# Optimization experiments

Hardware: AMD Instinct MI355X
Metric: run time of the kernel (lower is better)

Reference implementation:

```python
import math
import jax, jax.numpy as jnp
import numpy as np

B, N, D, H = 4, 2048, 1024, 16
DK = D // H

def setup_inputs() -> dict:
    key = jax.random.key(0)
    k1, k2, k3 = jax.random.split(key, 3)
    x = jax.random.normal(k1, (B, N, D), dtype=jnp.float32)
    # torch Linear weight is [out,in]; we store transposed [in,out] for x @ W
    w_qkv = jax.random.normal(k2, (D, 3 * D), dtype=jnp.float32) * (1.0 / math.sqrt(D))
    w_out = jax.random.normal(k3, (D, D), dtype=jnp.float32) * (1.0 / math.sqrt(D))
    return {"x": x, "w_qkv": w_qkv, "w_out": w_out}

def reference(x, w_qkv, w_out):
    b, n, d = x.shape
    qkv = x @ w_qkv                                   # [B,N,3D]
    q, k, v = jnp.split(qkv, 3, axis=-1)
    def split_heads(t):
        return t.reshape(b, n, H, DK).transpose(0, 2, 1, 3)  # [B,H,N,DK]
    q, k, v = map(split_heads, (q, k, v))
    scale = 1.0 / math.sqrt(DK)
    attn = jnp.einsum('bhqd,bhkd->bhqk', q, k) * scale  # [B,H,N,N]
    attn = jax.nn.softmax(attn, axis=-1)
    out = jnp.einsum('bhqk,bhkd->bhqd', attn, v)        # [B,H,N,DK]
    out = out.transpose(0, 2, 1, 3).reshape(b, n, d)
    return out @ w_out                                  # dropout p=0 -> identity
```

## Files before the change

### kernel.cpp

```cpp
#include <hip/hip_runtime.h>
#include <hip/hip_bf16.h>

typedef __bf16 bf16;
typedef __bf16 bf16x8 __attribute__((ext_vector_type(8)));
typedef float f32x2 __attribute__((ext_vector_type(2)));
typedef float f32x4 __attribute__((ext_vector_type(4)));
typedef float f32x16 __attribute__((ext_vector_type(16)));
typedef short s16x4 __attribute__((ext_vector_type(4)));

#define GLDS16(gp, lp) __builtin_amdgcn_global_load_lds( \
    (const __attribute__((address_space(1))) void*)(gp), \
    (__attribute__((address_space(3))) void*)(lp), 16, 0, 0)

__device__ __forceinline__ bf16 f2bf(float f) {
    unsigned u = __builtin_bit_cast(unsigned, f);
    u = (u + 0x7FFFu + ((u >> 16) & 1u)) >> 16;
    unsigned short s = (unsigned short)u;
    return __builtin_bit_cast(bf16, s);
}
__device__ __forceinline__ void store_c(float* p, float v) { *p = v; }
__device__ __forceinline__ void store_c(bf16*  p, float v) { *p = f2bf(v); }

__device__ __forceinline__ float exp2_fast(float x) {
    float r; asm("v_exp_f32 %0, %1" : "=v"(r) : "v"(x)); return r;
}
__device__ __forceinline__ unsigned cvt_pk_bf16(float lo, float hi) {
    unsigned r;
    asm("v_cvt_pk_bf16_f32 %0, %1, %2" : "=v"(r) : "v"(lo), "v"(hi));
    return r;
}
__device__ __forceinline__ void permlane32_swap(unsigned &a, unsigned &b) {
    asm("v_permlane32_swap_b32 %0, %1" : "+v"(a), "+v"(b));
}
__device__ __forceinline__ s16x4 ds_tr16(unsigned addr) {
    s16x4 d;
    asm volatile("ds_read_b64_tr_b16 %0, %1" : "=v"(d) : "v"(addr));
    return d;
}

__global__ __launch_bounds__(256) void cvt_f32_bf16(
    const float* __restrict__ in, bf16* __restrict__ out, int n8)
{
    int i = blockIdx.x * 256 + threadIdx.x;
    if (i >= n8) return;
    f32x4 a = *(const f32x4*)(in + (size_t)i * 8);
    f32x4 b = *(const f32x4*)(in + (size_t)i * 8 + 4);
    bf16x8 o;
    #pragma unroll
    for (int j = 0; j < 4; ++j) { o[j] = f2bf(a[j]); o[4 + j] = f2bf(b[j]); }
    *(bf16x8*)(out + (size_t)i * 8) = o;
}

template <typename TC>
__global__ __launch_bounds__(256) void gemm_glds(
    const bf16* __restrict__ A, const bf16* __restrict__ B, TC* __restrict__ C,
    int M, int N, int K)
{
    __shared__ alignas(16) bf16 As[128 * 32];
    __shared__ alignas(16) bf16 Bs[32 * 128];

    const int tid  = threadIdx.x;
    const int wv   = tid >> 6;
    const int lane = tid & 63;
    const int lr   = lane & 15;
    const int kb   = lane >> 4;
    const int wr   = wv >> 1, wc = wv & 1;
    const int brow = blockIdx.y * 128;
    const int bcol = blockIdx.x * 128;

    f32x4 acc[4][4] = {};

    const int ar0 = wv * 16 + (lane >> 2);
    const int ac0 = (lane & 3) * 8;

    const int bL   = wv * 1024 + lane * 16;
    const int bs0  = bL >> 7;
    const int b_r  = (bL & 127) >> 5;
    const int b_c0 = (bL & 31) >> 1;

    for (int k0 = 0; k0 < K; k0 += 32) {
        __syncthreads();
        #pragma unroll
        for (int t = 0; t < 2; ++t)
            GLDS16(A + (size_t)(brow + t * 64 + ar0) * K + k0 + ac0,
                   &As[t * 2048 + wv * 512]);
        #pragma unroll
        for (int t = 0; t < 2; ++t) {
            int s = bs0 + t * 32;
            GLDS16(B + (size_t)(k0 + (s >> 3) * 4 + b_r) * N + bcol + (s & 7) * 16 + b_c0,
                   &Bs[t * 2048 + wv * 512]);
        }
        __syncthreads();

        bf16x8 af[4], bfr[4];
        #pragma unroll
        for (int m = 0; m < 4; ++m)
            af[m] = *(const bf16x8*)&As[(wr * 64 + m * 16 + lr) * 32 + kb * 8];
        {
            s16x4 tr[8];
            const unsigned bsb = (unsigned)(uintptr_t)Bs + kb * 2048 + lr * 8;
            #pragma unroll
            for (int nt = 0; nt < 4; ++nt) {
                unsigned a = bsb + (wc * 4 + nt) * 128;
                tr[nt * 2]     = ds_tr16(a);
                tr[nt * 2 + 1] = ds_tr16(a + 1024);
            }
            asm volatile("s_waitcnt lgkmcnt(0)" ::: "memory");
            __builtin_amdgcn_sched_barrier(0);
            #pragma unroll
            for (int nt = 0; nt < 4; ++nt) {
                union { bf16x8 f; s16x4 h[2]; } u;
                u.h[0] = tr[nt * 2]; u.h[1] = tr[nt * 2 + 1];
                bfr[nt] = u.f;
            }
        }
        #pragma unroll
        for (int m = 0; m < 4; ++m)
            #pragma unroll
            for (int n = 0; n < 4; ++n)
                acc[m][n] = __builtin_amdgcn_mfma_f32_16x16x32_bf16(af[m], bfr[n], acc[m][n], 0, 0, 0);
    }

    #pragma unroll
    for (int m = 0; m < 4; ++m)
        #pragma unroll
        for (int n = 0; n < 4; ++n)
            #pragma unroll
            for (int r = 0; r < 4; ++r) {
                int row = brow + wr * 64 + m * 16 + kb * 4 + r;
                int col = bcol + wc * 64 + n * 16 + lr;
                store_c(&C[(size_t)row * N + col], acc[m][n][r]);
            }
}

__global__ __launch_bounds__(256) void attn_mfma32(
    const bf16* __restrict__ qkv, bf16* __restrict__ attn_out)
{
    constexpr int NSEQ = 2048, DM = 1024, LD = 3072, KVB = 64, QB = 128;
    constexpr int NT = NSEQ / KVB;
    constexpr float THR = 11.5f;
    __shared__ alignas(16) char smem[18432];
    bf16 (*Ks)[72] = (bf16 (*)[72])smem;
    bf16 *Vs       = (bf16*)(smem + 9216);
    bf16 (*Os)[72] = (bf16 (*)[72])smem;

    const int tid = threadIdx.x;
    const int wv = tid >> 6, lane = tid & 63;
    const int l31 = lane & 31;
    const int hi_ = lane >> 5;
    const int g16 = (lane >> 4) & 1;
    const int l16 = lane & 15;

    const int wg  = blockIdx.x;
    const int xcd = wg & 7, j = wg >> 3;
    const int bh  = xcd * 8 + (j & 7);
    const int q0  = (j >> 3) * QB;
    const int b = bh >> 4, h = bh & 15;

    const bf16* qbase = qkv + (size_t)(b * NSEQ) * LD + h * 64;
    const bf16* kbase = qbase + DM;
    const bf16* vbase = qbase + 2 * DM;

    bf16x8 qf[4];
    {
        const float QSC = 0.125f * 1.44269504f;
        const bf16* qp = qbase + (size_t)(q0 + wv * 32 + l31) * LD + hi_ * 8;
        #pragma unroll
        for (int ds = 0; ds < 4; ++ds) {
            bf16x8 t = *(const bf16x8*)(qp + ds * 16);
            #pragma unroll
            for (int e = 0; e < 8; ++e) t[e] = f2bf((float)t[e] * QSC);
            qf[ds] = t;
        }
    }

    f32x16 o0 = {}, o1 = {};
    float mrow = -INFINITY, lsum = 0.f;

    const int krow = tid >> 2, kcol = (tid & 3) * 16;
    const unsigned vb = (unsigned)(uintptr_t)Vs;

    auto vload = [&](int j0, int L) {
        int kq = L >> 8, cb = (L >> 6) & 3, rr = (L >> 4) & 3, c0 = L & 15;
        return *(const bf16x8*)(vbase + (size_t)(j0 + kq * 4 + rr) * LD + cb * 16 + c0);
    };

    bf16x8 kr0 = *(const bf16x8*)(kbase + (size_t)krow * LD + kcol);
    bf16x8 kr1 = *(const bf16x8*)(kbase + (size_t)krow * LD + kcol + 8);
    bf16x8 vr0 = vload(0, tid * 8);
    bf16x8 vr1 = vload(0, 2048 + tid * 8);

    for (int kt = 0; kt < NT; ++kt) {
        __syncthreads();
        *(bf16x8*)&Ks[krow][kcol]       = kr0;
        *(bf16x8*)&Ks[krow][kcol + 8]   = kr1;
        *(bf16x8*)(Vs + tid * 8)        = vr0;
        *(bf16x8*)(Vs + 2048 + tid * 8) = vr1;
        __syncthreads();

        {
            const int jn = (kt + 1 < NT ? kt + 1 : kt) * KVB;
            kr0 = *(const bf16x8*)(kbase + (size_t)(jn + krow) * LD + kcol);
            kr1 = *(const bf16x8*)(kbase + (size_t)(jn + krow) * LD + kcol + 8);
            vr0 = vload(jn, tid * 8);
            vr1 = vload(jn, 2048 + tid * 8);
        }

        f32x16 sT0 = {}, sT1 = {};
        __builtin_amdgcn_s_setprio(1);
        #pragma unroll
        for (int ds = 0; ds < 4; ++ds) {
            bf16x8 kf = *(const bf16x8*)&Ks[l31][ds * 16 + hi_ * 8];
            sT0 = __builtin_amdgcn_mfma_f32_32x32x16_bf16(kf, qf[ds], sT0, 0, 0, 0);
        }
        #pragma unroll
        for (int ds = 0; ds < 4; ++ds) {
            bf16x8 kf = *(const bf16x8*)&Ks[32 + l31][ds * 16 + hi_ * 8];
            sT1 = __builtin_amdgcn_mfma_f32_32x32x16_bf16(kf, qf[ds], sT1, 0, 0, 0);
        }
        __builtin_amdgcn_s_setprio(0);

        float pm = fmaxf(sT0[0], sT0[1]);
        #pragma unroll
        for (int r = 2; r < 16; r += 2) pm = fmaxf(fmaxf(pm, sT0[r]), sT0[r + 1]);
        #pragma unroll
        for (int r = 0; r < 16; r += 2) pm = fmaxf(fmaxf(pm, sT1[r]), sT1[r + 1]);
        pm = fmaxf(pm, __shfl_xor(pm, 32));
        if (!__all(pm <= mrow + THR)) {
            const float mn = fmaxf(mrow, pm);
            const float corr = exp2_fast(mrow - mn);
            mrow = mn;
            lsum *= corr;
            #pragma unroll
            for (int r = 0; r < 16; ++r) { o0[r] *= corr; o1[r] *= corr; }
        }
        #pragma unroll
        for (int r = 0; r < 16; ++r) sT0[r] = exp2_fast(sT0[r] - mrow);
        #pragma unroll
        for (int r = 0; r < 16; ++r) sT1[r] = exp2_fast(sT1[r] - mrow);
        f32x2 ps2 = {0.f, 0.f};
        #pragma unroll
        for (int r = 0; r < 16; r += 2) {
            ps2 += (f32x2){sT0[r], sT0[r + 1]};
            ps2 += (f32x2){sT1[r], sT1[r + 1]};
        }
        float ps = ps2[0] + ps2[1];
        ps += __shfl_xor(ps, 32);
        lsum += ps;

        unsigned w0[8], w1[8];
        #pragma unroll
        for (int j2 = 0; j2 < 8; ++j2) {
            w0[j2] = cvt_pk_bf16(sT0[2 * j2], sT0[2 * j2 + 1]);
            w1[j2] = cvt_pk_bf16(sT1[2 * j2], sT1[2 * j2 + 1]);
        }
        bf16x8 pf[4];
        #pragma unroll
        for (int ks = 0; ks < 4; ++ks) {
            const int jb = 4 * (ks & 1);
            unsigned a0 = (ks >> 1) ? w1[jb]     : w0[jb];
            unsigned b0 = (ks >> 1) ? w1[jb + 2] : w0[jb + 2];
            unsigned a1 = (ks >> 1) ? w1[jb + 1] : w0[jb + 1];
            unsigned b1 = (ks >> 1) ? w1[jb + 3] : w0[jb + 3];
            permlane32_swap(a0, b0);
            permlane32_swap(a1, b1);
            union { bf16x8 f; unsigned w[4]; } u;
            u.w[0] = a0; u.w[1] = a1; u.w[2] = b0; u.w[3] = b1;
            pf[ks] = u.f;
        }

        #pragma unroll
        for (int dt = 0; dt < 2; ++dt) {
            s16x4 t[8];
            #pragma unroll
            for (int ks = 0; ks < 4; ++ks) {
                unsigned a = vb + ks * 2048 + hi_ * 1024 + dt * 256 + g16 * 128 + l16 * 8;
                t[ks * 2]     = ds_tr16(a);
                t[ks * 2 + 1] = ds_tr16(a + 512);
            }
            asm volatile("s_waitcnt lgkmcnt(0)" ::: "memory");
            __builtin_amdgcn_sched_barrier(0);
            __builtin_amdgcn_s_setprio(1);
            #pragma unroll
            for (int ks = 0; ks < 4; ++ks) {
                union { bf16x8 f; s16x4 h[2]; } u;
                u.h[0] = t[ks * 2]; u.h[1] = t[ks * 2 + 1];
                if (dt == 0) o0 = __builtin_amdgcn_mfma_f32_32x32x16_bf16(u.f, pf[ks], o0, 0, 0, 0);
                else         o1 = __builtin_amdgcn_mfma_f32_32x32x16_bf16(u.f, pf[ks], o1, 0, 0, 0);
            }
            __builtin_amdgcn_s_setprio(0);
        }
    }

    const float inv = 1.f / lsum;
    __syncthreads();
    #pragma unroll
    for (int r = 0; r < 16; ++r) {
        const int d0 = (r & 3) + 8 * (r >> 2) + 4 * hi_;
        Os[wv * 32 + l31][d0]      = f2bf(o0[r] * inv);
        Os[wv * 32 + l31][32 + d0] = f2bf(o1[r] * inv);
    }
    __syncthreads();
    {
        const int row = tid >> 1, c0 = (tid & 1) * 32;
        bf16* op = attn_out + (size_t)(b * NSEQ + q0 + row) * DM + h * 64 + c0;
        #pragma unroll
        for (int e = 0; e < 4; ++e)
            *(bf16x8*)(op + e * 8) = *(const bf16x8*)&Os[row][c0 + e * 8];
    }
}

extern "C" void kernel_launch(void* const* d_in, const int* in_sizes, int n_in,
                              void* d_out, int out_size, void* d_ws, size_t ws_size,
                              hipStream_t stream) {
    const float* x     = (const float*)d_in[0];
    const float* w_qkv = (const float*)d_in[1];
    const float* w_out = (const float*)d_in[2];
    float* out = (float*)d_out;

    bf16* x_bf    = (bf16*)d_out;
    bf16* qkv     = (bf16*)d_ws;
    bf16* wqkv_bf = qkv + (size_t)8192 * 3072;
    bf16* attnb   = wqkv_bf;
    bf16* wo_bf   = (bf16*)d_ws;

    cvt_f32_bf16<<<4096, 256, 0, stream>>>(x, x_bf, 8192 * 1024 / 8);
    cvt_f32_bf16<<<1536, 256, 0, stream>>>(w_qkv, wqkv_bf, 1024 * 3072 / 8);
    gemm_glds<bf16><<<dim3(3072 / 128, 8192 / 128), 256, 0, stream>>>(
        x_bf, wqkv_bf, qkv, 8192, 3072, 1024);
    attn_mfma32<<<1024, 256, 0, stream>>>(qkv, attnb);
    cvt_f32_bf16<<<512, 256, 0, stream>>>(w_out, wo_bf, 1024 * 1024 / 8);
    gemm_glds<float><<<dim3(1024 / 128, 8192 / 128), 256, 0, stream>>>(
        attnb, wo_bf, out, 8192, 1024, 1024);
}
```

Baseline: 222.2 us.

## Add 256x256 double-buffered 8-wave GEMM for QKV projection

Adds a new bf16 GEMM kernel with 256x256 block tiles, 512 threads, K-step 64, and double-buffered LDS. The global-to-LDS loads for the next tile are spread across the MFMA phases of the current one, B fragments are read with transposing LDS loads, A tiles use an XOR swizzle, and blocks are remapped for L2 locality. The QKV projection now uses it instead of the 128x128 kernel, aiming at more data reuse and overlap of loads with compute. The cost is large LDS use (128KB per block, with two blocks per CU requested) and heavy register pressure from the 8x4 accumulators, which can limit occupancy.

```diff
diff --git a/kernel.cpp b/kernel.cpp
--- a/kernel.cpp
+++ b/kernel.cpp
@@ -52,6 +52,138 @@
 }
 
 template <typename TC>
+__global__ __launch_bounds__(512, 2) void gemm_8ph(
+    const bf16* __restrict__ A, const bf16* __restrict__ B, TC* __restrict__ C,
+    int M, int N, int K)
+{
+    __shared__ alignas(16) bf16 Al[2][256 * 64];
+    __shared__ alignas(16) bf16 Bl[2][64 * 256];
+
+    const int tid  = threadIdx.x;
+    const int wv   = tid >> 6;
+    const int lane = tid & 63;
+    const int lr   = lane & 15;
+    const int kb   = lane >> 4;
+    const int wm   = wv >> 2, wn = wv & 3;
+
+    const int nbx = N >> 8;
+    int id = (int)blockIdx.x;
+    id = (id & 7) * ((int)gridDim.x >> 3) + (id >> 3);
+    const int brow = (id / nbx) * 256, bcol = (id % nbx) * 256;
+
+    const int aRow  = wv * 8 + (lane >> 3);
+    const int aSlot = (lane & 7) ^ ((lane >> 3) & 7);
+    const int bL0 = wv * 1024 + lane * 16;
+    const int bS0 = bL0 >> 7;
+    const int bR  = (bL0 & 127) >> 5;
+    const int bC0 = (bL0 & 31) >> 1;
+
+    f32x4 acc[8][4] = {};
+
+    auto stageA = [&](int buf, int k0, int t) {
+        GLDS16(A + (size_t)(brow + t * 64 + aRow) * K + k0 + aSlot * 8,
+               &Al[buf][t * 4096 + wv * 512]);
+    };
+    auto stageB = [&](int buf, int k0, int t) {
+        int s = bS0 + t * 64;
+        GLDS16(B + (size_t)(k0 + (s >> 4) * 4 + bR) * N + bcol + (s & 15) * 16 + bC0,
+               &Bl[buf][t * 4096 + wv * 512]);
+    };
+    auto ldA = [&](const bf16* Ab, int m, int ks) {
+        int row = wm * 128 + m * 16 + lr;
+        int off = row * 128 + ((ks * 64 + kb * 16) ^ ((lr & 7) << 4));
+        return *(const bf16x8*)((const char*)Ab + off);
+    };
+
+    #pragma unroll
+    for (int t = 0; t < 4; ++t) { stageA(0, 0, t); stageB(0, 0, t); }
+    __syncthreads();
+
+    const int KT = K >> 6;
+    for (int kt = 0; kt < KT; ++kt) {
+        const int cur = kt & 1, nxt = cur ^ 1;
+        const bf16* Ab = Al[cur];
+        const unsigned bB = (unsigned)(uintptr_t)Bl[cur];
+        const int nk0 = (kt + 1) << 6;
+        const bool doStage = (kt + 1 < KT);
+
+        if (doStage) { stageA(nxt, nk0, 0); stageA(nxt, nk0, 1); }
+        s16x4 btr[4][2][2];
+        #pragma unroll
+        for (int nt = 0; nt < 4; ++nt)
+            #pragma unroll
+            for (int ks = 0; ks < 2; ++ks) {
+                unsigned a = bB + (unsigned)((ks * 8 + kb * 2) * 2048 + (wn * 4 + nt) * 128 + lr * 8);
+                btr[nt][ks][0] = ds_tr16(a);
+                btr[nt][ks][1] = ds_tr16(a + 2048);
+            }
+        bf16x8 af0[2][2];
+        #pragma unroll
+        for (int m = 0; m < 2; ++m)
+            #pragma unroll
+            for (int ks = 0; ks < 2; ++ks) af0[m][ks] = ldA(Ab, m, ks);
+        asm volatile("s_waitcnt lgkmcnt(0)" ::: "memory");
+        __builtin_amdgcn_sched_barrier(0);
+        bf16x8 bfr[4][2];
+        #pragma unroll
+        for (int nt = 0; nt < 4; ++nt)
+            #pragma unroll
+            for (int ks = 0; ks < 2; ++ks) {
+                union { bf16x8 f; s16x4 h[2]; } u;
+                u.h[0] = btr[nt][ks][0]; u.h[1] = btr[nt][ks][1];
+                bfr[nt][ks] = u.f;
+            }
+        __builtin_amdgcn_s_setprio(1);
+        #pragma unroll
+        for (int m = 0; m < 2; ++m)
+            #pragma unroll
+            for (int nt = 0; nt < 4; ++nt)
+                #pragma unroll
+                for (int ks = 0; ks < 2; ++ks)
+                    acc[m][nt] = __builtin_amdgcn_mfma_f32_16x16x32_bf16(
+                        af0[m][ks], bfr[nt][ks], acc[m][nt], 0, 0, 0);
+        __builtin_amdgcn_s_setprio(0);
+
+        #pragma unroll
+        for (int mq = 1; mq < 4; ++mq) {
+            if (doStage) {
+                if (mq == 1) { stageA(nxt, nk0, 2); stageA(nxt, nk0, 3); }
+                if (mq == 2) { stageB(nxt, nk0, 0); stageB(nxt, nk0, 1); }
+                if (mq == 3) { stageB(nxt, nk0, 2); stageB(nxt, nk0, 3); }
+            }
+            bf16x8 af[2][2];
+            #pragma unroll
+            for (int m = 0; m < 2; ++m)
+                #pragma unroll
+                for (int ks = 0; ks < 2; ++ks) af[m][ks] = ldA(Ab, mq * 2 + m, ks);
+            __builtin_amdgcn_s_setprio(1);
+            #pragma unroll
+            for (int m = 0; m < 2; ++m)
+                #pragma unroll
+                for (int nt = 0; nt < 4; ++nt)
+                    #pragma unroll
+                    for (int ks = 0; ks < 2; ++ks)
+                        acc[mq * 2 + m][nt] = __builtin_amdgcn_mfma_f32_16x16x32_bf16(
+                            af[m][ks], bfr[nt][ks], acc[mq * 2 + m][nt], 0, 0, 0);
+            __builtin_amdgcn_s_setprio(0);
+        }
+
+        __syncthreads();
+    }
+
+    #pragma unroll
+    for (int m = 0; m < 8; ++m)
+        #pragma unroll
+        for (int n = 0; n < 4; ++n)
+            #pragma unroll
+            for (int r = 0; r < 4; ++r) {
+                int row = brow + wm * 128 + m * 16 + kb * 4 + r;
+                int col = bcol + wn * 64 + n * 16 + lr;
+                store_c(&C[(size_t)row * N + col], acc[m][n][r]);
+            }
+}
+
+template <typename TC>
 __global__ __launch_bounds__(256) void gemm_glds(
     const bf16* __restrict__ A, const bf16* __restrict__ B, TC* __restrict__ C,
     int M, int N, int K)
@@ -326,7 +458,7 @@
 
     cvt_f32_bf16<<<4096, 256, 0, stream>>>(x, x_bf, 8192 * 1024 / 8);
     cvt_f32_bf16<<<1536, 256, 0, stream>>>(w_qkv, wqkv_bf, 1024 * 3072 / 8);
-    gemm_glds<bf16><<<dim3(3072 / 128, 8192 / 128), 256, 0, stream>>>(
+    gemm_8ph<bf16><<<(8192 / 256) * (3072 / 256), 512, 0, stream>>>(
         x_bf, wqkv_bf, qkv, 8192, 3072, 1024);
     attn_mfma32<<<1024, 256, 0, stream>>>(qkv, attnb);
     cvt_f32_bf16<<<512, 256, 0, stream>>>(w_out, wo_bf, 1024 * 1024 / 8);
```

Measured after the change: 238.0 us. 1.07x slower.
